# Performance work log

Hardware: AMD Instinct MI355X
Metric: run time of the kernel (lower is better)

The kernel has to match this reference:

```python
import jax, jax.numpy as jnp
import numpy as np

L, B, S, D, H, E, DH, K = 2, 4, 1024, 512, 8, 8, 2048, 2
HEAD = D // H
EPS = 1e-6


def setup_inputs() -> dict:
    key = jax.random.key(0)
    ks = jax.random.split(key, 10)
    s = 0.02
    rn = lambda k, shp: (s * jax.random.normal(k, shp, jnp.float32))
    return {
        "x": jax.random.normal(ks[0], (B, S, D), jnp.float32),
        "ln1_w": jnp.ones((L, D), jnp.float32),
        "ln1_b": jnp.zeros((L, D), jnp.float32),
        "wq": rn(ks[1], (L, D, D)),
        "wk": rn(ks[2], (L, D, D)),
        "wv": rn(ks[3], (L, D, D)),
        "wo": rn(ks[4], (L, D, D)),
        "bo": jnp.zeros((L, D), jnp.float32),
        "ln2_w": jnp.ones((L, D), jnp.float32),
        "ln2_b": jnp.zeros((L, D), jnp.float32),
        "gate_w": rn(ks[5], (L, D, E)),
        "w1": rn(ks[6], (L, E, D, DH)),
        "b1": jnp.zeros((L, E, DH), jnp.float32),
        "w2": rn(ks[7], (L, E, DH, D)),
        "b2": jnp.zeros((L, E, D), jnp.float32),
    }


def _layer_norm(x, w, b):
    mu = jnp.mean(x, axis=-1, keepdims=True)
    var = jnp.mean(jnp.square(x - mu), axis=-1, keepdims=True)
    return (x - mu) * jax.lax.rsqrt(var + EPS) * w + b


def _attention(h, wq_l, wk_l, wv_l, wo_l, bo_l):
    # h: [B,S,D] -> multi-head qk attention (attn_mode='qk'), dropout is eval (identity)
    q = (h @ wq_l).reshape(B, S, H, HEAD)
    k = (h @ wk_l).reshape(B, S, H, HEAD)
    v = (h @ wv_l).reshape(B, S, H, HEAD)
    attn = jnp.einsum('bqhd,bkhd->bhqk', q, k) / np.sqrt(HEAD).astype(np.float32)
    attn = jax.nn.softmax(attn, axis=-1)
    out = jnp.einsum('bhqk,bkhd->bqhd', attn, v).reshape(B, S, D)
    return out @ wo_l + bo_l


def _moe_ffn(x2d, gw, w1_l, b1_l, w2_l, b2_l):
    # x2d: [T,D]; top-k noisy-vmoe gate at eval: clean logits, softmax over the top-k logits
    logits = x2d @ gw  # [T,E]
    topv, topi = jax.lax.top_k(logits, K)  # [T,K]
    gates = jax.nn.softmax(topv, axis=-1)  # [T,K]
    T = x2d.shape[0]
    combine = jnp.zeros((T, E), x2d.dtype).at[jnp.arange(T)[:, None], topi].add(gates)  # [T,E]
    # dense grouped-expert MLP (exact erf GELU as torch.nn.GELU)
    hmid = jax.nn.gelu(jnp.einsum('td,edh->teh', x2d, w1_l) + b1_l[None], approximate=False)
    y = jnp.einsum('teh,ehd->ted', hmid, w2_l) + b2_l[None]
    return jnp.einsum('te,ted->td', combine, y)


def reference(x, ln1_w, ln1_b, wq, wk, wv, wo, bo, ln2_w, ln2_b, gate_w, w1, b1, w2, b2):
    for l in range(L):
        residue = x
        h = _layer_norm(x, ln1_w[l], ln1_b[l])
        x = _attention(h, wq[l], wk[l], wv[l], wo[l], bo[l]) + residue
        residue = x
        h = _layer_norm(x, ln2_w[l], ln2_b[l])
        y = _moe_ffn(h.reshape(B * S, D), gate_w[l], w1[l], b1[l], w2[l], b2[l])
        x = y.reshape(B, S, D) + residue
    return x
```

## Files before the change

kernel.cpp:

```cpp
#include <hip/hip_runtime.h>
#include <cmath>

#define D_MODEL 512
#define T_TOK   4096
#define S_SEQ   1024
#define DH_FF   2048
#define N_EXP   8
#define CAP     9216
#define QKV_LD  1536

typedef __attribute__((ext_vector_type(8))) short bf16x8_t;
typedef __attribute__((ext_vector_type(4))) float f32x4_t;
typedef _Float16 f16x8 __attribute__((ext_vector_type(8)));

__device__ __forceinline__ float gelu_exact(float x) {
    return 0.5f * x * (1.0f + erff(x * 0.70710678118654752440f));
}
__device__ __forceinline__ unsigned short f2bf(float f) {
    union { float f; unsigned int u; } v; v.f = f;
    unsigned int r = v.u + 0x7fff + ((v.u >> 16) & 1);
    return (unsigned short)(r >> 16);
}
__device__ __forceinline__ float bf2f(unsigned short u) {
    union { unsigned int i; float f; } v; v.i = ((unsigned int)u) << 16; return v.f;
}
__device__ __forceinline__ unsigned short f2h(float f) {
    _Float16 h = (_Float16)f;
    return __builtin_bit_cast(unsigned short, h);
}
__device__ __forceinline__ void split1(float v, unsigned short& h, unsigned short& l) {
    _Float16 hf = (_Float16)v;
    _Float16 lf = (_Float16)(v - (float)hf);
    h = __builtin_bit_cast(unsigned short, hf);
    l = __builtin_bit_cast(unsigned short, lf);
}

__global__ __launch_bounds__(256) void ln_kernel(
    const float* __restrict__ x, const float* __restrict__ w,
    const float* __restrict__ b, float* __restrict__ outf,
    unsigned short* __restrict__ outHi, unsigned short* __restrict__ outLo,
    unsigned short* __restrict__ outb, float* __restrict__ xcopy)
{
    const int t = blockIdx.x, tid = threadIdx.x;
    const float* xr = x + (size_t)t * D_MODEL;
    float v0 = xr[tid], v1 = xr[tid + 256];
    __shared__ float ss[256], sq[256];
    ss[tid] = v0 + v1;
    sq[tid] = v0 * v0 + v1 * v1;
    __syncthreads();
    for (int st = 128; st > 0; st >>= 1) {
        if (tid < st) { ss[tid] += ss[tid + st]; sq[tid] += sq[tid + st]; }
        __syncthreads();
    }
    float mu  = ss[0] * (1.0f / 512.0f);
    float var = sq[0] * (1.0f / 512.0f) - mu * mu;
    float rs  = rsqrtf(var + 1e-6f);
    float o0 = (v0 - mu) * rs * w[tid]       + b[tid];
    float o1 = (v1 - mu) * rs * w[tid + 256] + b[tid + 256];
    if (outf) {
        float* outr = outf + (size_t)t * D_MODEL;
        outr[tid] = o0; outr[tid + 256] = o1;
    }
    if (outHi) {
        unsigned short h0, l0, h1, l1;
        split1(o0, h0, l0); split1(o1, h1, l1);
        unsigned short* oh = outHi + (size_t)t * D_MODEL;
        unsigned short* ol = outLo + (size_t)t * D_MODEL;
        oh[tid] = h0; oh[tid + 256] = h1;
        ol[tid] = l0; ol[tid + 256] = l1;
    }
    if (outb) {
        unsigned short* ob = outb + (size_t)t * D_MODEL;
        ob[tid] = f2bf(o0); ob[tid + 256] = f2bf(o1);
    }
    if (xcopy) {
        float* xc = xcopy + (size_t)t * D_MODEL;
        xc[tid] = v0; xc[tid + 256] = v1;
    }
}

__global__ __launch_bounds__(256) void tconv_split(
    const float* __restrict__ in, int inLd, size_t eStrideIn,
    unsigned short* __restrict__ outHi, unsigned short* __restrict__ outLo,
    int outLd, size_t eStrideOut)
{
    __shared__ float Ts[32][33];
    const int tid = threadIdx.x;
    const int k0 = blockIdx.y * 32, n0 = blockIdx.x * 32;
    in    += (size_t)blockIdx.z * eStrideIn;
    outHi += (size_t)blockIdx.z * eStrideOut;
    outLo += (size_t)blockIdx.z * eStrideOut;
    int r = tid >> 3, c = (tid & 7) * 4;
    float4 v = *(const float4*)&in[(size_t)(k0 + r) * inLd + n0 + c];
    Ts[r][c] = v.x; Ts[r][c + 1] = v.y; Ts[r][c + 2] = v.z; Ts[r][c + 3] = v.w;
    __syncthreads();
    int n = tid >> 3, kk = (tid & 7) * 4;
    ushort4 h4, l4;
    split1(Ts[kk][n],     h4.x, l4.x); split1(Ts[kk + 1][n], h4.y, l4.y);
    split1(Ts[kk + 2][n], h4.z, l4.z); split1(Ts[kk + 3][n], h4.w, l4.w);
    size_t o = (size_t)(n0 + n) * outLd + k0 + kk;
    *(ushort4*)&outHi[o] = h4;
    *(ushort4*)&outLo[o] = l4;
}

__global__ __launch_bounds__(256) void tconv(
    const float* __restrict__ in, int inLd, size_t eStrideIn,
    unsigned short* __restrict__ out, int outLd, size_t eStrideOut)
{
    __shared__ float Ts[32][33];
    const int tid = threadIdx.x;
    const int k0 = blockIdx.y * 32, n0 = blockIdx.x * 32;
    in  += (size_t)blockIdx.z * eStrideIn;
    out += (size_t)blockIdx.z * eStrideOut;
    int r = tid >> 3, c = (tid & 7) * 4;
    float4 v = *(const float4*)&in[(size_t)(k0 + r) * inLd + n0 + c];
    Ts[r][c] = v.x; Ts[r][c + 1] = v.y; Ts[r][c + 2] = v.z; Ts[r][c + 3] = v.w;
    __syncthreads();
    int n = tid >> 3, kk = (tid & 7) * 4;
    ushort4 o;
    o.x = f2bf(Ts[kk][n]);     o.y = f2bf(Ts[kk + 1][n]);
    o.z = f2bf(Ts[kk + 2][n]); o.w = f2bf(Ts[kk + 3][n]);
    *(ushort4*)&out[(size_t)(n0 + n) * outLd + k0 + kk] = o;
}

template<int MODE>
__global__ __launch_bounds__(256) void gemm_pre(
    const unsigned short* __restrict__ Ahi, const unsigned short* __restrict__ Alo,
    int lda, int KLEN,
    const unsigned short* __restrict__ Bhi, const unsigned short* __restrict__ Blo,
    size_t BeStride,
    float* __restrict__ C, int ldc,
    const float* __restrict__ bias, int biasStride,
    const float* __restrict__ resid,
    const int* __restrict__ offs, const int* __restrict__ rowtok, int beta,
    unsigned short* __restrict__ Chi, unsigned short* __restrict__ Clo)
{
    __shared__ unsigned short As_hi[64][40], As_lo[64][40];
    __shared__ unsigned short Bs_hi[64][40], Bs_lo[64][40];
    __shared__ int rt[64];
    __shared__ float rg[64];
    const int tid = threadIdx.x;
    const int row0 = blockIdx.y * 64, col0 = blockIdx.x * 64;
    int e = 0;
    if (MODE == 2 || MODE == 5) {
        #pragma unroll
        for (int i = 1; i < N_EXP; i++) if (offs[i] <= row0) e = i;
        if (tid < 64) rt[tid] = rowtok[row0 + tid];
        if (MODE == 5 && tid >= 64 && tid < 128) rg[tid - 64] = resid[row0 + tid - 64];
        __syncthreads();
    }
    const unsigned short* BeH = Bhi + (size_t)e * BeStride;
    const unsigned short* BeL = Blo + (size_t)e * BeStride;
    const int lane = tid & 63, w = tid >> 6;
    const int wrow = (w >> 1) * 32, wcol = (w & 1) * 32;
    const int m_ = lane & 15, q_ = lane >> 4;
    f32x4_t acc[2][2];
    #pragma unroll
    for (int i = 0; i < 2; i++)
        #pragma unroll
        for (int j = 0; j < 2; j++) acc[i][j] = (f32x4_t){0.f, 0.f, 0.f, 0.f};

    const int sr = tid >> 2, sc = (tid & 3) * 8;
    size_t arow;
    bool azero = false;
    if (MODE == 2) {
        int t = rt[sr];
        azero = (t < 0);
        arow = (size_t)(azero ? 0 : t) * lda;
    } else {
        arow = (size_t)(row0 + sr) * lda;
    }
    const size_t brow = (size_t)(col0 + sr) * KLEN;

    for (int k0 = 0; k0 < KLEN; k0 += 32) {
        uint4 vh = azero ? make_uint4(0u, 0u, 0u, 0u) : *(const uint4*)&Ahi[arow + k0 + sc];
        uint4 vl = azero ? make_uint4(0u, 0u, 0u, 0u) : *(const uint4*)&Alo[arow + k0 + sc];
        *(uint4*)&As_hi[sr][sc] = vh;
        *(uint4*)&As_lo[sr][sc] = vl;
        *(uint4*)&Bs_hi[sr][sc] = *(const uint4*)&BeH[brow + k0 + sc];
        *(uint4*)&Bs_lo[sr][sc] = *(const uint4*)&BeL[brow + k0 + sc];
        __syncthreads();
        f16x8 ah[2], al[2], bh[2], bl[2];
        #pragma unroll
        for (int i = 0; i < 2; i++) {
            int r = wrow + 16 * i + m_;
            ah[i] = *(const f16x8*)&As_hi[r][q_ * 8];
            al[i] = *(const f16x8*)&As_lo[r][q_ * 8];
        }
        #pragma unroll
        for (int j = 0; j < 2; j++) {
            int r = wcol + 16 * j + m_;
            bh[j] = *(const f16x8*)&Bs_hi[r][q_ * 8];
            bl[j] = *(const f16x8*)&Bs_lo[r][q_ * 8];
        }
        #pragma unroll
        for (int i = 0; i < 2; i++)
            #pragma unroll
            for (int j = 0; j < 2; j++) {
                acc[i][j] = __builtin_amdgcn_mfma_f32_16x16x32_f16(ah[i], bl[j], acc[i][j], 0, 0, 0);
                acc[i][j] = __builtin_amdgcn_mfma_f32_16x16x32_f16(al[i], bh[j], acc[i][j], 0, 0, 0);
                acc[i][j] = __builtin_amdgcn_mfma_f32_16x16x32_f16(ah[i], bh[j], acc[i][j], 0, 0, 0);
            }
        __syncthreads();
    }
    #pragma unroll
    for (int i = 0; i < 2; i++) {
        #pragma unroll
        for (int j = 0; j < 2; j++) {
            #pragma unroll
            for (int r = 0; r < 4; r++) {
                int lr = wrow + 16 * i + q_ * 4 + r;
                int gr = row0 + lr;
                int gc = col0 + wcol + 16 * j + m_;
                float v = acc[i][j][r];
                if (MODE == 5) {
                    int t = rt[lr];
                    if (t >= 0) {
                        float add = beta ? bias[(size_t)e * biasStride + gc] : 0.0f;
                        atomicAdd(&C[(size_t)t * ldc + gc], rg[lr] * (v + add));
                    }
                } else if (MODE == 2) {
                    float g = gelu_exact(v + bias[(size_t)e * biasStride + gc]);
                    unsigned short gh, gl;
                    split1(g, gh, gl);
                    size_t idx = (size_t)gr * ldc + gc;
                    Chi[idx] = gh; Clo[idx] = gl;
                } else {
                    size_t idx = (size_t)gr * ldc + gc;
                    if (MODE == 1) C[idx] = v + bias[gc] + resid[idx];
                    else           C[idx] = v;
                }
            }
        }
    }
}

template<int MODE>
__global__ __launch_bounds__(256) void gemm_pre_bt(
    const unsigned short* __restrict__ A, int lda, int KLEN,
    const unsigned short* __restrict__ Bt, size_t BeStride,
    unsigned short* __restrict__ C, int ldc,
    const float* __restrict__ biasBase, int biasStride,
    const int* __restrict__ offs, const int* __restrict__ rowtok,
    const float* __restrict__ rowgate, float* __restrict__ Cout, int beta)
{
    __shared__ unsigned short As[64][72];
    __shared__ unsigned short Bs[64][72];
    __shared__ int rt[64];
    __shared__ float rg[64];
    const int tid = threadIdx.x;
    const int row0 = blockIdx.y * 64, col0 = blockIdx.x * 64;
    int e = 0;
    #pragma unroll
    for (int i = 1; i < N_EXP; i++) if (offs[i] <= row0) e = i;
    if (tid < 64) rt[tid] = rowtok[row0 + tid];
    if (MODE == 5 && tid >= 64 && tid < 128) rg[tid - 64] = rowgate[row0 + tid - 64];
    __syncthreads();
    const unsigned short* Be = Bt + (size_t)e * BeStride;
    const int lane = tid & 63, w = tid >> 6;
    const int wrow = (w >> 1) * 32, wcol = (w & 1) * 32;
    const int m_ = lane & 15, q_ = lane >> 4;
    f32x4_t acc[2][2];
    #pragma unroll
    for (int i = 0; i < 2; i++)
        #pragma unroll
        for (int j = 0; j < 2; j++) acc[i][j] = (f32x4_t){0.f, 0.f, 0.f, 0.f};

    const int sr = tid >> 3, sc = (tid & 7) * 8;
    size_t arow0, arow1;
    bool az0 = false, az1 = false;
    {
        int r1 = sr + 32;
        if (MODE == 2) {
            int t0 = rt[sr], t1 = rt[r1];
            az0 = (t0 < 0); az1 = (t1 < 0);
            arow0 = (size_t)(az0 ? 0 : t0) * lda;
            arow1 = (size_t)(az1 ? 0 : t1) * lda;
        } else {
            arow0 = (size_t)(row0 + sr) * lda;
            arow1 = (size_t)(row0 + r1) * lda;
        }
    }
    const size_t brow0 = (size_t)(col0 + sr) * KLEN;
    const size_t brow1 = (size_t)(col0 + sr + 32) * KLEN;

    for (int k0 = 0; k0 < KLEN; k0 += 64) {
        uint4 a0 = az0 ? make_uint4(0u, 0u, 0u, 0u) : *(const uint4*)&A[arow0 + k0 + sc];
        uint4 a1 = az1 ? make_uint4(0u, 0u, 0u, 0u) : *(const uint4*)&A[arow1 + k0 + sc];
        *(uint4*)&As[sr][sc]      = a0;
        *(uint4*)&As[sr + 32][sc] = a1;
        *(uint4*)&Bs[sr][sc]      = *(const uint4*)&Be[brow0 + k0 + sc];
        *(uint4*)&Bs[sr + 32][sc] = *(const uint4*)&Be[brow1 + k0 + sc];
        __syncthreads();
        #pragma unroll
        for (int ks = 0; ks < 2; ks++) {
            bf16x8_t af[2], bfr[2];
            #pragma unroll
            for (int i = 0; i < 2; i++)
                af[i] = *(const bf16x8_t*)&As[wrow + 16 * i + m_][ks * 32 + q_ * 8];
            #pragma unroll
            for (int j = 0; j < 2; j++)
                bfr[j] = *(const bf16x8_t*)&Bs[wcol + 16 * j + m_][ks * 32 + q_ * 8];
            #pragma unroll
            for (int i = 0; i < 2; i++)
                #pragma unroll
                for (int j = 0; j < 2; j++)
                    acc[i][j] = __builtin_amdgcn_mfma_f32_16x16x32_bf16(
                        af[i], bfr[j], acc[i][j], 0, 0, 0);
        }
        __syncthreads();
    }
    #pragma unroll
    for (int i = 0; i < 2; i++) {
        #pragma unroll
        for (int j = 0; j < 2; j++) {
            #pragma unroll
            for (int r = 0; r < 4; r++) {
                int lr = wrow + 16 * i + q_ * 4 + r;
                int gr = row0 + lr;
                int gc = col0 + wcol + 16 * j + m_;
                float v = acc[i][j][r];
                if (MODE == 5) {
                    int t = rt[lr];
                    if (t >= 0) {
                        float add = beta ? biasBase[(size_t)e * biasStride + gc] : 0.0f;
                        atomicAdd(&Cout[(size_t)t * ldc + gc], rg[lr] * (v + add));
                    }
                } else {
                    C[(size_t)gr * ldc + gc] =
                        f2bf(gelu_exact(v + biasBase[(size_t)e * biasStride + gc]));
                }
            }
        }
    }
}

__global__ __launch_bounds__(256) void qkv_prep(
    const float* __restrict__ qkvb, unsigned short* __restrict__ Qh,
    unsigned short* __restrict__ Kh, unsigned short* __restrict__ VTh)
{
    __shared__ float Ts[64][65];
    const int tid = threadIdx.x;
    const int t0 = blockIdx.x * 64, hh = blockIdx.y, b = blockIdx.z;
    const int bh = b * 8 + hh;
    const float* src = qkvb + ((size_t)(b * S_SEQ + t0)) * QKV_LD + hh * 64;
    #pragma unroll
    for (int i = 0; i < 4; i++) {
        int flat = tid + i * 256;
        int r = flat >> 4, c4 = (flat & 15) * 4;
        float4 qv = *(const float4*)&src[(size_t)r * QKV_LD + c4];
        float4 kv = *(const float4*)&src[(size_t)r * QKV_LD + 512 + c4];
        float4 vv = *(const float4*)&src[(size_t)r * QKV_LD + 1024 + c4];
        ushort4 qo, ko;
        qo.x = f2h(qv.x * 0.125f); qo.y = f2h(qv.y * 0.125f);
        qo.z = f2h(qv.z * 0.125f); qo.w = f2h(qv.w * 0.125f);
        ko.x = f2h(kv.x); ko.y = f2h(kv.y); ko.z = f2h(kv.z); ko.w = f2h(kv.w);
        size_t o = ((size_t)bh * S_SEQ + t0 + r) * 64 + c4;
        *(ushort4*)&Qh[o] = qo;
        *(ushort4*)&Kh[o] = ko;
        Ts[r][c4] = vv.x; Ts[r][c4 + 1] = vv.y; Ts[r][c4 + 2] = vv.z; Ts[r][c4 + 3] = vv.w;
    }
    __syncthreads();
    #pragma unroll
    for (int i = 0; i < 4; i++) {
        int flat = tid + i * 256;
        int d = flat >> 4, s4 = (flat & 15) * 4;
        ushort4 vo;
        vo.x = f2h(Ts[s4][d]);     vo.y = f2h(Ts[s4 + 1][d]);
        vo.z = f2h(Ts[s4 + 2][d]); vo.w = f2h(Ts[s4 + 3][d]);
        *(ushort4*)&VTh[((size_t)bh * 64 + d) * S_SEQ + t0 + s4] = vo;
    }
}

__global__ __launch_bounds__(256) void flash_attn_mfma(
    const unsigned short* __restrict__ Qh, const unsigned short* __restrict__ Kh,
    const unsigned short* __restrict__ VTh,
    unsigned short* __restrict__ outHi, unsigned short* __restrict__ outLo)
{
    __shared__ unsigned short Ks[64 * 72];
    __shared__ unsigned short Vt[64 * 72];
    __shared__ unsigned short Ps[64 * 72];
    const int tid = threadIdx.x;
    const int lane = tid & 63, w = tid >> 6;
    const int m_ = lane & 15, q_ = lane >> 4;
    const int hh = blockIdx.y, b = blockIdx.z;
    const int bh = b * 8 + hh;
    const int q0 = blockIdx.x * 64;
    const size_t qbase = ((size_t)bh * S_SEQ + q0) * 64;
    const size_t kbase = (size_t)bh * S_SEQ * 64;
    const size_t vbase = (size_t)bh * 64 * S_SEQ;

    f16x8 qa[2];
    #pragma unroll
    for (int c = 0; c < 2; c++)
        qa[c] = *(const f16x8*)&Qh[qbase + (size_t)(w * 16 + m_) * 64 + c * 32 + q_ * 8];

    float m_run[4], l_run[4];
    f32x4_t acc[4];
    #pragma unroll
    for (int r = 0; r < 4; r++) { m_run[r] = -INFINITY; l_run[r] = 0.0f; }
    #pragma unroll
    for (int oj = 0; oj < 4; oj++) acc[oj] = (f32x4_t){0.f, 0.f, 0.f, 0.f};

    for (int kv0 = 0; kv0 < S_SEQ; kv0 += 64) {
        __syncthreads();
        #pragma unroll
        for (int i = 0; i < 2; i++) {
            int g = tid + i * 256;
            int r = g >> 3, c8 = (g & 7) * 8;
            *(uint4*)&Ks[r * 72 + c8] =
                *(const uint4*)&Kh[kbase + (size_t)(kv0 + r) * 64 + c8];
            *(uint4*)&Vt[r * 72 + c8] =
                *(const uint4*)&VTh[vbase + (size_t)r * S_SEQ + kv0 + c8];
        }
        __syncthreads();
        f32x4_t s[4];
        #pragma unroll
        for (int j = 0; j < 4; j++) s[j] = (f32x4_t){0.f, 0.f, 0.f, 0.f};
        #pragma unroll
        for (int c = 0; c < 2; c++)
            #pragma unroll
            for (int j = 0; j < 4; j++) {
                f16x8 kb = *(const f16x8*)&Ks[(j * 16 + m_) * 72 + c * 32 + q_ * 8];
                s[j] = __builtin_amdgcn_mfma_f32_16x16x32_f16(qa[c], kb, s[j], 0, 0, 0);
            }
        float alpha[4];
        #pragma unroll
        for (int r = 0; r < 4; r++) {
            float rm = fmaxf(fmaxf(s[0][r], s[1][r]), fmaxf(s[2][r], s[3][r]));
            #pragma unroll
            for (int mk = 1; mk < 16; mk <<= 1)
                rm = fmaxf(rm, __shfl_xor(rm, mk));
            float mn = fmaxf(m_run[r], rm);
            alpha[r] = __expf(m_run[r] - mn);
            m_run[r] = mn;
            float ps = 0.0f;
            #pragma unroll
            for (int j = 0; j < 4; j++) {
                float p = __expf(s[j][r] - mn);
                s[j][r] = p;
                ps += p;
            }
            #pragma unroll
            for (int mk = 1; mk < 16; mk <<= 1)
                ps += __shfl_xor(ps, mk);
            l_run[r] = l_run[r] * alpha[r] + ps;
        }
        #pragma unroll
        for (int oj = 0; oj < 4; oj++)
            #pragma unroll
            for (int r = 0; r < 4; r++)
                acc[oj][r] *= alpha[r];
        #pragma unroll
        for (int j = 0; j < 4; j++)
            #pragma unroll
            for (int r = 0; r < 4; r++)
                Ps[(w * 16 + q_ * 4 + r) * 72 + j * 16 + m_] = f2h(s[j][r]);
        __syncthreads();
        #pragma unroll
        for (int c = 0; c < 2; c++) {
            f16x8 pa = *(const f16x8*)&Ps[(w * 16 + m_) * 72 + c * 32 + q_ * 8];
            #pragma unroll
            for (int oj = 0; oj < 4; oj++) {
                f16x8 vb = *(const f16x8*)&Vt[(oj * 16 + m_) * 72 + c * 32 + q_ * 8];
                acc[oj] = __builtin_amdgcn_mfma_f32_16x16x32_f16(pa, vb, acc[oj], 0, 0, 0);
            }
        }
    }
    const size_t obase = ((size_t)b * S_SEQ + q0) * D_MODEL + hh * 64;
    #pragma unroll
    for (int r = 0; r < 4; r++) {
        float inv = 1.0f / l_run[r];
        #pragma unroll
        for (int oj = 0; oj < 4; oj++) {
            float v = acc[oj][r] * inv;
            unsigned short vh, vl;
            split1(v, vh, vl);
            size_t idx = obase + (size_t)(w * 16 + q_ * 4 + r) * D_MODEL + oj * 16 + m_;
            outHi[idx] = vh;
            outLo[idx] = vl;
        }
    }
}

__global__ __launch_bounds__(256) void gate_kernel(
    const float* __restrict__ h, const float* __restrict__ gw,
    int* __restrict__ topi, float* __restrict__ gates)
{
    const int w = threadIdx.x >> 6, lane = threadIdx.x & 63;
    const int t = blockIdx.x * 4 + w;
    const float* hr = h + (size_t)t * D_MODEL;
    float acc[N_EXP] = {};
    for (int d = lane; d < D_MODEL; d += 64) {
        float xv = hr[d];
        const float4 g0 = *(const float4*)&gw[(size_t)d * N_EXP];
        const float4 g1 = *(const float4*)&gw[(size_t)d * N_EXP + 4];
        acc[0] += xv * g0.x; acc[1] += xv * g0.y;
        acc[2] += xv * g0.z; acc[3] += xv * g0.w;
        acc[4] += xv * g1.x; acc[5] += xv * g1.y;
        acc[6] += xv * g1.z; acc[7] += xv * g1.w;
    }
    #pragma unroll
    for (int mk = 1; mk < 64; mk <<= 1) {
        #pragma unroll
        for (int e = 0; e < N_EXP; e++) acc[e] += __shfl_xor(acc[e], mk);
    }
    if (lane == 0) {
        int e0 = 0; float v0 = acc[0];
        #pragma unroll
        for (int e = 1; e < N_EXP; e++) if (acc[e] > v0) { v0 = acc[e]; e0 = e; }
        int e1 = -1; float v1 = -INFINITY;
        #pragma unroll
        for (int e = 0; e < N_EXP; e++) if (e != e0 && acc[e] > v1) { v1 = acc[e]; e1 = e; }
        float g0 = 1.0f / (1.0f + __expf(v1 - v0));
        float g1 = 1.0f - g0;
        topi[2 * t] = e0; topi[2 * t + 1] = e1;
        gates[2 * t] = g0; gates[2 * t + 1] = g1;
    }
}

__global__ __launch_bounds__(1024) void route_kernel(
    const int* __restrict__ topi, const float* __restrict__ gates,
    int* __restrict__ offs, int* __restrict__ rowtok, float* __restrict__ rowgate)
{
    __shared__ int wcnt[16][N_EXP];
    __shared__ int wbase[16][N_EXP];
    __shared__ int offs_s[N_EXP + 1];
    const int tid = threadIdx.x, w = tid >> 6, lane = tid & 63;
    const unsigned long long lt = (1ULL << lane) - 1ULL;

    int mye[8];
    int cnt[N_EXP] = {};
    #pragma unroll
    for (int r = 0; r < 8; r++) {
        int i = w * 512 + r * 64 + lane;
        int e = topi[i];
        mye[r] = e;
        #pragma unroll
        for (int e8 = 0; e8 < N_EXP; e8++) {
            unsigned long long m = __ballot(e == e8);
            cnt[e8] += (int)__popcll(m);
        }
    }
    if (lane == 0) {
        #pragma unroll
        for (int e8 = 0; e8 < N_EXP; e8++) wcnt[w][e8] = cnt[e8];
    }
    __syncthreads();
    if (tid == 0) {
        int off = 0;
        for (int e8 = 0; e8 < N_EXP; e8++) {
            offs_s[e8] = off;
            int c = 0;
            for (int ww = 0; ww < 16; ww++) c += wcnt[ww][e8];
            off += (c + 127) & ~127;
        }
        offs_s[N_EXP] = off;
        for (int e8 = 0; e8 <= N_EXP; e8++) offs[e8] = offs_s[e8];
    }
    __syncthreads();
    if (tid < 128) {
        int ww = tid >> 3, e8 = tid & 7;
        int bse = offs_s[e8];
        for (int w2 = 0; w2 < ww; w2++) bse += wcnt[w2][e8];
        wbase[ww][e8] = bse;
    }
    __syncthreads();
    int base[N_EXP];
    #pragma unroll
    for (int e8 = 0; e8 < N_EXP; e8++) base[e8] = wbase[w][e8];
    #pragma unroll
    for (int r = 0; r < 8; r++) {
        int i = w * 512 + r * 64 + lane;
        int e = mye[r];
        int pos = 0;
        #pragma unroll
        for (int e8 = 0; e8 < N_EXP; e8++) {
            unsigned long long m = __ballot(e == e8);
            if (e == e8) pos = base[e8] + (int)__popcll(m & lt);
            base[e8] += (int)__popcll(m);
        }
        rowtok[pos] = i >> 1;
        rowgate[pos] = gates[i];
    }
}

extern "C" void kernel_launch(void* const* d_in, const int* in_sizes, int n_in,
                              void* d_out, int out_size, void* d_ws, size_t ws_size,
                              hipStream_t stream)
{
    const float* x0    = (const float*)d_in[0];
    const float* ln1w  = (const float*)d_in[1];
    const float* ln1b  = (const float*)d_in[2];
    const float* wq    = (const float*)d_in[3];
    const float* wk    = (const float*)d_in[4];
    const float* wv    = (const float*)d_in[5];
    const float* wo    = (const float*)d_in[6];
    const float* bo    = (const float*)d_in[7];
    const float* ln2w  = (const float*)d_in[8];
    const float* ln2b  = (const float*)d_in[9];
    const float* gatew = (const float*)d_in[10];
    const float* w1    = (const float*)d_in[11];
    const float* b1    = (const float*)d_in[12];
    const float* w2    = (const float*)d_in[13];
    const float* b2    = (const float*)d_in[14];
    float* out = (float*)d_out;

    char* ws = (char*)d_ws;
    const size_t MiB = 1 << 20;
    unsigned short* Qh    = (unsigned short*)(ws + 0);
    unsigned short* Kh    = (unsigned short*)(ws + 4 * MiB);
    unsigned short* h_hi  = (unsigned short*)(ws + 8 * MiB);
    unsigned short* h_lo  = (unsigned short*)(ws + 12 * MiB);
    unsigned short* attn_hi = (unsigned short*)(ws + 8 * MiB);
    unsigned short* attn_lo = (unsigned short*)(ws + 12 * MiB);
    float* qkvb = (float*)(ws + 16 * MiB);
    float* x1   = (float*)(ws + 16 * MiB);
    unsigned short* wqkvT_hi = (unsigned short*)(ws + 40 * MiB);
    unsigned short* wqkvT_lo = (unsigned short*)(ws + 40 * MiB + QKV_LD * D_MODEL * 2);
    unsigned short* VTh   = (unsigned short*)(ws + 40 * MiB);
    unsigned short* woT_hi = (unsigned short*)(ws + 44 * MiB);
    unsigned short* woT_lo = (unsigned short*)(ws + 44 * MiB + D_MODEL * D_MODEL * 2);
    unsigned short* h2_hi = (unsigned short*)(ws + 0);
    unsigned short* h2_lo = (unsigned short*)(ws + 4 * MiB);
    unsigned short* h2b   = (unsigned short*)(ws + 0);
    float* h2 = (float*)(ws + 8 * MiB);
    unsigned short* w1T_hi = (unsigned short*)(ws + 8 * MiB);
    unsigned short* w1T_lo = (unsigned short*)(ws + 12 * MiB);
    unsigned short* w2T_hi = (unsigned short*)(ws + 16 * MiB);
    unsigned short* w2T_lo = (unsigned short*)(ws + 20 * MiB);
    unsigned short* hmid_hi = (unsigned short*)(ws + 24 * MiB);
    unsigned short* hmid_lo = (unsigned short*)(ws + 33 * MiB);
    unsigned short* w1T_bf  = (unsigned short*)(ws + 8 * MiB);
    unsigned short* w2T_bf  = (unsigned short*)(ws + 16 * MiB);
    unsigned short* hmidb   = (unsigned short*)(ws + 24 * MiB);
    size_t oI = 46 * MiB;
    int*   topi    = (int*)(ws + oI);
    float* gates   = (float*)(ws + oI + 2 * T_TOK * 4);
    int*   rowtok  = (int*)(ws + oI + 4 * T_TOK * 4);
    float* rowgate = (float*)(ws + oI + 4 * T_TOK * 4 + CAP * 4);
    int*   offs    = (int*)(ws + oI + 4 * T_TOK * 4 + 2 * CAP * 4);
    float* x2 = out;

    const dim3 gW(16, 16, 1);
    const dim3 gW8(16, 16, 8);
    const dim3 gW8b(16, 32, 8);
    const dim3 gQKV(QKV_LD / 64, T_TOK / 64);
    const dim3 gO(D_MODEL / 64, T_TOK / 64);
    const dim3 gUp1(8, CAP / 64);
    const dim3 gDn1(D_MODEL / 64, CAP / 64);
    const dim3 gUp2(16, CAP / 64);
    const dim3 gDn2(D_MODEL / 64, CAP / 64);
    const dim3 gAttn(S_SEQ / 64, 8, 4);

    for (int l = 0; l < 2; l++) {
        const float* xin = (l == 0) ? x0 : x2;
        float* xout = (l == 1) ? out : x2;
        const float* wq_l = wq + (size_t)l * D_MODEL * D_MODEL;
        const float* wk_l = wk + (size_t)l * D_MODEL * D_MODEL;
        const float* wv_l = wv + (size_t)l * D_MODEL * D_MODEL;
        const float* wo_l = wo + (size_t)l * D_MODEL * D_MODEL;
        const float* w1_l = w1 + (size_t)l * N_EXP * D_MODEL * DH_FF;
        const float* w2_l = w2 + (size_t)l * N_EXP * DH_FF * D_MODEL;
        const float* b1_l = b1 + (size_t)l * N_EXP * DH_FF;
        const float* b2_l = b2 + (size_t)l * N_EXP * D_MODEL;

        ln_kernel<<<T_TOK, 256, 0, stream>>>(xin, ln1w + (size_t)l * D_MODEL,
                                             ln1b + (size_t)l * D_MODEL,
                                             nullptr, h_hi, h_lo, nullptr, nullptr);
        tconv_split<<<gW, 256, 0, stream>>>(wq_l, D_MODEL, 0, wqkvT_hi, wqkvT_lo, D_MODEL, 0);
        tconv_split<<<gW, 256, 0, stream>>>(wk_l, D_MODEL, 0,
                                            wqkvT_hi + 512 * 512, wqkvT_lo + 512 * 512,
                                            D_MODEL, 0);
        tconv_split<<<gW, 256, 0, stream>>>(wv_l, D_MODEL, 0,
                                            wqkvT_hi + 1024 * 512, wqkvT_lo + 1024 * 512,
                                            D_MODEL, 0);
        tconv_split<<<gW, 256, 0, stream>>>(wo_l, D_MODEL, 0, woT_hi, woT_lo, D_MODEL, 0);
        gemm_pre<0><<<gQKV, 256, 0, stream>>>(h_hi, h_lo, D_MODEL, D_MODEL,
                                              wqkvT_hi, wqkvT_lo, 0,
                                              qkvb, QKV_LD, nullptr, 0, nullptr,
                                              nullptr, nullptr, 0, nullptr, nullptr);
        qkv_prep<<<gAttn, 256, 0, stream>>>(qkvb, Qh, Kh, VTh);
        flash_attn_mfma<<<gAttn, 256, 0, stream>>>(Qh, Kh, VTh, attn_hi, attn_lo);
        gemm_pre<1><<<gO, 256, 0, stream>>>(attn_hi, attn_lo, D_MODEL, D_MODEL,
                                            woT_hi, woT_lo, 0,
                                            x1, D_MODEL, bo + (size_t)l * D_MODEL, 0,
                                            xin, nullptr, nullptr, 0, nullptr, nullptr);
        ln_kernel<<<T_TOK, 256, 0, stream>>>(x1, ln2w + (size_t)l * D_MODEL,
                                             ln2b + (size_t)l * D_MODEL, h2,
                                             (l == 0) ? h2_hi : nullptr,
                                             (l == 0) ? h2_lo : nullptr,
                                             (l == 1) ? h2b : nullptr, xout);

        hipMemsetAsync(rowtok, 0xFF, CAP * 4, stream);
        gate_kernel<<<T_TOK / 4, 256, 0, stream>>>(h2, gatew + (size_t)l * D_MODEL * N_EXP,
                                                   topi, gates);
        route_kernel<<<1, 1024, 0, stream>>>(topi, gates, offs, rowtok, rowgate);

        if (l == 0) {
            for (int c = 0; c < 4; c++) {
                tconv_split<<<gW8, 256, 0, stream>>>(w1_l + (size_t)c * 512, DH_FF,
                                                     (size_t)D_MODEL * DH_FF,
                                                     w1T_hi, w1T_lo, D_MODEL,
                                                     (size_t)512 * D_MODEL);
                gemm_pre<2><<<gUp1, 256, 0, stream>>>(h2_hi, h2_lo, D_MODEL, D_MODEL,
                                                      w1T_hi, w1T_lo, (size_t)512 * D_MODEL,
                                                      nullptr, 512,
                                                      b1_l + (size_t)c * 512, DH_FF,
                                                      nullptr, offs, rowtok, 0,
                                                      hmid_hi, hmid_lo);
                tconv_split<<<gW8, 256, 0, stream>>>(w2_l + (size_t)c * 512 * D_MODEL,
                                                     D_MODEL, (size_t)DH_FF * D_MODEL,
                                                     w2T_hi, w2T_lo, 512,
                                                     (size_t)D_MODEL * 512);
                gemm_pre<5><<<gDn1, 256, 0, stream>>>(hmid_hi, hmid_lo, 512, 512,
                                                      w2T_hi, w2T_lo, (size_t)D_MODEL * 512,
                                                      xout, D_MODEL, b2_l, D_MODEL,
                                                      rowgate, offs, rowtok,
                                                      (c == 0) ? 1 : 0, nullptr, nullptr);
            }
        } else {
            for (int c = 0; c < 2; c++) {
                tconv<<<dim3(32, 16, 8), 256, 0, stream>>>(
                    w1_l + (size_t)c * 1024, DH_FF, (size_t)D_MODEL * DH_FF,
                    w1T_bf, D_MODEL, (size_t)1024 * D_MODEL);
                gemm_pre_bt<2><<<gUp2, 256, 0, stream>>>(h2b, D_MODEL, D_MODEL,
                                                         w1T_bf, (size_t)1024 * D_MODEL,
                                                         hmidb, 1024,
                                                         b1_l + (size_t)c * 1024, DH_FF,
                                                         offs, rowtok, nullptr, nullptr, 0);
                tconv<<<dim3(16, 32, 8), 256, 0, stream>>>(
                    w2_l + (size_t)c * 1024 * D_MODEL, D_MODEL, (size_t)DH_FF * D_MODEL,
                    w2T_bf, 1024, (size_t)D_MODEL * 1024);
                gemm_pre_bt<5><<<gDn2, 256, 0, stream>>>(hmidb, 1024, 1024,
                                                         w2T_bf, (size_t)D_MODEL * 1024,
                                                         nullptr, D_MODEL, b2_l, D_MODEL,
                                                         offs, rowtok, rowgate, xout,
                                                         (c == 0) ? 1 : 0);
            }
        }
    }
}
```

Before: 922.1 us.

## Enlarge GEMM tiles to 128 rows and prefetch next K-slice into registers

Both GEMM kernels (split-precision f16 and bf16) now use 128-row block tiles with templated 64- or 128-column widths, and each wave computes more MFMA output tiles. This raises data reuse per LDS load and cuts the number of blocks. The K loop now loads the next global slice into registers while the current slice is being computed, which removes one barrier per iteration. The cost is higher register pressure and fewer blocks in flight, which may lower occupancy. For the MoE expert GEMMs, a 128-row tile may also cross expert boundaries if the routing offsets are not 128-aligned.

Measured after the change: 1.567 ms. 69.9% more time.

```diff
diff --git a/kernel.cpp b/kernel.cpp
--- a/kernel.cpp
+++ b/kernel.cpp
@@ -123,8 +123,8 @@
     *(ushort4*)&out[(size_t)(n0 + n) * outLd + k0 + kk] = o;
 }
 
-template<int MODE>
-__global__ __launch_bounds__(256) void gemm_pre(
+template<int MODE, int BN>
+__global__ __launch_bounds__(256) void gemm128(
     const unsigned short* __restrict__ Ahi, const unsigned short* __restrict__ Alo,
     int lda, int KLEN,
     const unsigned short* __restrict__ Bhi, const unsigned short* __restrict__ Blo,
@@ -135,78 +135,108 @@
     const int* __restrict__ offs, const int* __restrict__ rowtok, int beta,
     unsigned short* __restrict__ Chi, unsigned short* __restrict__ Clo)
 {
-    __shared__ unsigned short As_hi[64][40], As_lo[64][40];
-    __shared__ unsigned short Bs_hi[64][40], Bs_lo[64][40];
-    __shared__ int rt[64];
-    __shared__ float rg[64];
+    constexpr int NI  = (BN == 64) ? 2 : 4;
+    constexpr int NBV = BN / 64;
+    __shared__ unsigned short AsH[128][40], AsL[128][40];
+    __shared__ unsigned short BsH[BN][40],  BsL[BN][40];
+    __shared__ int rt[128];
+    __shared__ float rg[128];
     const int tid = threadIdx.x;
-    const int row0 = blockIdx.y * 64, col0 = blockIdx.x * 64;
+    const int row0 = blockIdx.y * 128, col0 = blockIdx.x * BN;
     int e = 0;
     if (MODE == 2 || MODE == 5) {
         #pragma unroll
         for (int i = 1; i < N_EXP; i++) if (offs[i] <= row0) e = i;
-        if (tid < 64) rt[tid] = rowtok[row0 + tid];
-        if (MODE == 5 && tid >= 64 && tid < 128) rg[tid - 64] = resid[row0 + tid - 64];
+        if (tid < 128) rt[tid] = rowtok[row0 + tid];
+        else if (MODE == 5) rg[tid - 128] = resid[row0 + tid - 128];
         __syncthreads();
     }
     const unsigned short* BeH = Bhi + (size_t)e * BeStride;
     const unsigned short* BeL = Blo + (size_t)e * BeStride;
     const int lane = tid & 63, w = tid >> 6;
-    const int wrow = (w >> 1) * 32, wcol = (w & 1) * 32;
+    const int wrow = (BN == 64) ? w * 32 : (w >> 1) * 64;
+    const int wcol = (BN == 64) ? 0 : (w & 1) * 64;
     const int m_ = lane & 15, q_ = lane >> 4;
-    f32x4_t acc[2][2];
-    #pragma unroll
-    for (int i = 0; i < 2; i++)
-        #pragma unroll
-        for (int j = 0; j < 2; j++) acc[i][j] = (f32x4_t){0.f, 0.f, 0.f, 0.f};
-
-    const int sr = tid >> 2, sc = (tid & 3) * 8;
-    size_t arow;
-    bool azero = false;
-    if (MODE == 2) {
-        int t = rt[sr];
-        azero = (t < 0);
-        arow = (size_t)(azero ? 0 : t) * lda;
-    } else {
-        arow = (size_t)(row0 + sr) * lda;
-    }
-    const size_t brow = (size_t)(col0 + sr) * KLEN;
-
-    for (int k0 = 0; k0 < KLEN; k0 += 32) {
-        uint4 vh = azero ? make_uint4(0u, 0u, 0u, 0u) : *(const uint4*)&Ahi[arow + k0 + sc];
-        uint4 vl = azero ? make_uint4(0u, 0u, 0u, 0u) : *(const uint4*)&Alo[arow + k0 + sc];
-        *(uint4*)&As_hi[sr][sc] = vh;
-        *(uint4*)&As_lo[sr][sc] = vl;
-        *(uint4*)&Bs_hi[sr][sc] = *(const uint4*)&BeH[brow + k0 + sc];
-        *(uint4*)&Bs_lo[sr][sc] = *(const uint4*)&BeL[brow + k0 + sc];
+    f32x4_t acc[NI][4];
+    #pragma unroll
+    for (int i = 0; i < NI; i++)
+        #pragma unroll
+        for (int j = 0; j < 4; j++) acc[i][j] = (f32x4_t){0.f, 0.f, 0.f, 0.f};
+
+    const int ar0 = tid >> 2, ac = (tid & 3) * 8;
+    size_t aoff[2]; bool az[2];
+    #pragma unroll
+    for (int q = 0; q < 2; q++) {
+        int r = q * 64 + ar0;
+        if (MODE == 2) {
+            int t = rt[r];
+            az[q] = (t < 0);
+            aoff[q] = (size_t)(az[q] ? 0 : t) * lda;
+        } else { az[q] = false; aoff[q] = (size_t)(row0 + r) * lda; }
+    }
+    size_t boff[NBV];
+    #pragma unroll
+    for (int q = 0; q < NBV; q++)
+        boff[q] = (size_t)(col0 + q * 64 + ar0) * KLEN;
+
+    const uint4 Z = make_uint4(0u, 0u, 0u, 0u);
+    uint4 pah[2], pal[2], pbh[NBV], pbl[NBV];
+    auto LOAD = [&](int k0) {
+        #pragma unroll
+        for (int q = 0; q < 2; q++) {
+            pah[q] = az[q] ? Z : *(const uint4*)&Ahi[aoff[q] + k0 + ac];
+            pal[q] = az[q] ? Z : *(const uint4*)&Alo[aoff[q] + k0 + ac];
+        }
+        #pragma unroll
+        for (int q = 0; q < NBV; q++) {
+            pbh[q] = *(const uint4*)&BeH[boff[q] + k0 + ac];
+            pbl[q] = *(const uint4*)&BeL[boff[q] + k0 + ac];
+        }
+    };
+    auto STORE = [&]() {
+        #pragma unroll
+        for (int q = 0; q < 2; q++) {
+            *(uint4*)&AsH[q * 64 + ar0][ac] = pah[q];
+            *(uint4*)&AsL[q * 64 + ar0][ac] = pal[q];
+        }
+        #pragma unroll
+        for (int q = 0; q < NBV; q++) {
+            *(uint4*)&BsH[q * 64 + ar0][ac] = pbh[q];
+            *(uint4*)&BsL[q * 64 + ar0][ac] = pbl[q];
+        }
+    };
+
+    const int NS = KLEN / 32;
+    LOAD(0);
+    for (int ks = 0; ks < NS; ks++) {
+        if (ks) __syncthreads();
+        STORE();
+        if (ks + 1 < NS) LOAD(32 * (ks + 1));
         __syncthreads();
-        f16x8 ah[2], al[2], bh[2], bl[2];
-        #pragma unroll
-        for (int i = 0; i < 2; i++) {
+        f16x8 ah[NI], al[NI];
+        #pragma unroll
+        for (int i = 0; i < NI; i++) {
             int r = wrow + 16 * i + m_;
-            ah[i] = *(const f16x8*)&As_hi[r][q_ * 8];
-            al[i] = *(const f16x8*)&As_lo[r][q_ * 8];
-        }
-        #pragma unroll
-        for (int j = 0; j < 2; j++) {
+            ah[i] = *(const f16x8*)&AsH[r][q_ * 8];
+            al[i] = *(const f16x8*)&AsL[r][q_ * 8];
+        }
+        #pragma unroll
+        for (int j = 0; j < 4; j++) {
             int r = wcol + 16 * j + m_;
-            bh[j] = *(const f16x8*)&Bs_hi[r][q_ * 8];
-            bl[j] = *(const f16x8*)&Bs_lo[r][q_ * 8];
-        }
-        #pragma unroll
-        for (int i = 0; i < 2; i++)
-            #pragma unroll
-            for (int j = 0; j < 2; j++) {
-                acc[i][j] = __builtin_amdgcn_mfma_f32_16x16x32_f16(ah[i], bl[j], acc[i][j], 0, 0, 0);
-                acc[i][j] = __builtin_amdgcn_mfma_f32_16x16x32_f16(al[i], bh[j], acc[i][j], 0, 0, 0);
-                acc[i][j] = __builtin_amdgcn_mfma_f32_16x16x32_f16(ah[i], bh[j], acc[i][j], 0, 0, 0);
-            }
-        __syncthreads();
-    }
-    #pragma unroll
-    for (int i = 0; i < 2; i++) {
-        #pragma unroll
-        for (int j = 0; j < 2; j++) {
+            f16x8 bh = *(const f16x8*)&BsH[r][q_ * 8];
+            f16x8 bl = *(const f16x8*)&BsL[r][q_ * 8];
+            #pragma unroll
+            for (int i = 0; i < NI; i++) {
+                acc[i][j] = __builtin_amdgcn_mfma_f32_16x16x32_f16(ah[i], bl, acc[i][j], 0, 0, 0);
+                acc[i][j] = __builtin_amdgcn_mfma_f32_16x16x32_f16(al[i], bh, acc[i][j], 0, 0, 0);
+                acc[i][j] = __builtin_amdgcn_mfma_f32_16x16x32_f16(ah[i], bh, acc[i][j], 0, 0, 0);
+            }
+        }
+    }
+    #pragma unroll
+    for (int i = 0; i < NI; i++) {
+        #pragma unroll
+        for (int j = 0; j < 4; j++) {
             #pragma unroll
             for (int r = 0; r < 4; r++) {
                 int lr = wrow + 16 * i + q_ * 4 + r;
@@ -235,8 +265,8 @@
     }
 }
 
-template<int MODE>
-__global__ __launch_bounds__(256) void gemm_pre_bt(
+template<int MODE, int BN>
+__global__ __launch_bounds__(256) void gemm128_bt(
     const unsigned short* __restrict__ A, int lda, int KLEN,
     const unsigned short* __restrict__ Bt, size_t BeStride,
     unsigned short* __restrict__ C, int ldc,
@@ -244,76 +274,93 @@
     const int* __restrict__ offs, const int* __restrict__ rowtok,
     const float* __restrict__ rowgate, float* __restrict__ Cout, int beta)
 {
-    __shared__ unsigned short As[64][72];
-    __shared__ unsigned short Bs[64][72];
-    __shared__ int rt[64];
-    __shared__ float rg[64];
+    constexpr int NI  = (BN == 64) ? 2 : 4;
+    constexpr int NBV = BN / 32;
+    __shared__ unsigned short As[128][72];
+    __shared__ unsigned short Bs[BN][72];
+    __shared__ int rt[128];
+    __shared__ float rg[128];
     const int tid = threadIdx.x;
-    const int row0 = blockIdx.y * 64, col0 = blockIdx.x * 64;
+    const int row0 = blockIdx.y * 128, col0 = blockIdx.x * BN;
     int e = 0;
     #pragma unroll
     for (int i = 1; i < N_EXP; i++) if (offs[i] <= row0) e = i;
-    if (tid < 64) rt[tid] = rowtok[row0 + tid];
-    if (MODE == 5 && tid >= 64 && tid < 128) rg[tid - 64] = rowgate[row0 + tid - 64];
+    if (tid < 128) rt[tid] = rowtok[row0 + tid];
+    else if (MODE == 5) rg[tid - 128] = rowgate[row0 + tid - 128];
     __syncthreads();
     const unsigned short* Be = Bt + (size_t)e * BeStride;
     const int lane = tid & 63, w = tid >> 6;
-    const int wrow = (w >> 1) * 32, wcol = (w & 1) * 32;
+    const int wrow = (BN == 64) ? w * 32 : (w >> 1) * 64;
+    const int wcol = (BN == 64) ? 0 : (w & 1) * 64;
     const int m_ = lane & 15, q_ = lane >> 4;
-    f32x4_t acc[2][2];
-    #pragma unroll
-    for (int i = 0; i < 2; i++)
-        #pragma unroll
-        for (int j = 0; j < 2; j++) acc[i][j] = (f32x4_t){0.f, 0.f, 0.f, 0.f};
-
-    const int sr = tid >> 3, sc = (tid & 7) * 8;
-    size_t arow0, arow1;
-    bool az0 = false, az1 = false;
-    {
-        int r1 = sr + 32;
+    f32x4_t acc[NI][4];
+    #pragma unroll
+    for (int i = 0; i < NI; i++)
+        #pragma unroll
+        for (int j = 0; j < 4; j++) acc[i][j] = (f32x4_t){0.f, 0.f, 0.f, 0.f};
+
+    const int ar0 = tid >> 3, ac = (tid & 7) * 8;
+    size_t aoff[4]; bool az[4];
+    #pragma unroll
+    for (int q = 0; q < 4; q++) {
+        int r = q * 32 + ar0;
         if (MODE == 2) {
-            int t0 = rt[sr], t1 = rt[r1];
-            az0 = (t0 < 0); az1 = (t1 < 0);
-            arow0 = (size_t)(az0 ? 0 : t0) * lda;
-            arow1 = (size_t)(az1 ? 0 : t1) * lda;
-        } else {
-            arow0 = (size_t)(row0 + sr) * lda;
-            arow1 = (size_t)(row0 + r1) * lda;
-        }
-    }
-    const size_t brow0 = (size_t)(col0 + sr) * KLEN;
-    const size_t brow1 = (size_t)(col0 + sr + 32) * KLEN;
-
-    for (int k0 = 0; k0 < KLEN; k0 += 64) {
-        uint4 a0 = az0 ? make_uint4(0u, 0u, 0u, 0u) : *(const uint4*)&A[arow0 + k0 + sc];
-        uint4 a1 = az1 ? make_uint4(0u, 0u, 0u, 0u) : *(const uint4*)&A[arow1 + k0 + sc];
-        *(uint4*)&As[sr][sc]      = a0;
-        *(uint4*)&As[sr + 32][sc] = a1;
-        *(uint4*)&Bs[sr][sc]      = *(const uint4*)&Be[brow0 + k0 + sc];
-        *(uint4*)&Bs[sr + 32][sc] = *(const uint4*)&Be[brow1 + k0 + sc];
+            int t = rt[r];
+            az[q] = (t < 0);
+            aoff[q] = (size_t)(az[q] ? 0 : t) * lda;
+        } else { az[q] = false; aoff[q] = (size_t)(row0 + r) * lda; }
+    }
+    size_t boff[NBV];
+    #pragma unroll
+    for (int q = 0; q < NBV; q++)
+        boff[q] = (size_t)(col0 + q * 32 + ar0) * KLEN;
+
+    const uint4 Z = make_uint4(0u, 0u, 0u, 0u);
+    uint4 pa[4], pb[NBV];
+    auto LOAD = [&](int k0) {
+        #pragma unroll
+        for (int q = 0; q < 4; q++)
+            pa[q] = az[q] ? Z : *(const uint4*)&A[aoff[q] + k0 + ac];
+        #pragma unroll
+        for (int q = 0; q < NBV; q++)
+            pb[q] = *(const uint4*)&Be[boff[q] + k0 + ac];
+    };
+    auto STORE = [&]() {
+        #pragma unroll
+        for (int q = 0; q < 4; q++)
+            *(uint4*)&As[q * 32 + ar0][ac] = pa[q];
+        #pragma unroll
+        for (int q = 0; q < NBV; q++)
+            *(uint4*)&Bs[q * 32 + ar0][ac] = pb[q];
+    };
+
+    const int NS = KLEN / 64;
+    LOAD(0);
+    for (int ks = 0; ks < NS; ks++) {
+        if (ks) __syncthreads();
+        STORE();
+        if (ks + 1 < NS) LOAD(64 * (ks + 1));
         __syncthreads();
         #pragma unroll
-        for (int ks = 0; ks < 2; ks++) {
-            bf16x8_t af[2], bfr[2];
-            #pragma unroll
-            for (int i = 0; i < 2; i++)
-                af[i] = *(const bf16x8_t*)&As[wrow + 16 * i + m_][ks * 32 + q_ * 8];
-            #pragma unroll
-            for (int j = 0; j < 2; j++)
-                bfr[j] = *(const bf16x8_t*)&Bs[wcol + 16 * j + m_][ks * 32 + q_ * 8];
-            #pragma unroll
-            for (int i = 0; i < 2; i++)
+        for (int ks2 = 0; ks2 < 2; ks2++) {
+            bf16x8_t af[NI];
+            #pragma unroll
+            for (int i = 0; i < NI; i++)
+                af[i] = *(const bf16x8_t*)&As[wrow + 16 * i + m_][ks2 * 32 + q_ * 8];
+            #pragma unroll
+            for (int j = 0; j < 4; j++) {
+                bf16x8_t bfr = *(const bf16x8_t*)&Bs[wcol + 16 * j + m_][ks2 * 32 + q_ * 8];
                 #pragma unroll
-                for (int j = 0; j < 2; j++)
+                for (int i = 0; i < NI; i++)
                     acc[i][j] = __builtin_amdgcn_mfma_f32_16x16x32_bf16(
-                        af[i], bfr[j], acc[i][j], 0, 0, 0);
-        }
-        __syncthreads();
-    }
-    #pragma unroll
-    for (int i = 0; i < 2; i++) {
-        #pragma unroll
-        for (int j = 0; j < 2; j++) {
+                        af[i], bfr, acc[i][j], 0, 0, 0);
+            }
+        }
+    }
+    #pragma unroll
+    for (int i = 0; i < NI; i++) {
+        #pragma unroll
+        for (int j = 0; j < 4; j++) {
             #pragma unroll
             for (int r = 0; r < 4; r++) {
                 int lr = wrow + 16 * i + q_ * 4 + r;
@@ -644,13 +691,12 @@
 
     const dim3 gW(16, 16, 1);
     const dim3 gW8(16, 16, 8);
-    const dim3 gW8b(16, 32, 8);
-    const dim3 gQKV(QKV_LD / 64, T_TOK / 64);
-    const dim3 gO(D_MODEL / 64, T_TOK / 64);
-    const dim3 gUp1(8, CAP / 64);
-    const dim3 gDn1(D_MODEL / 64, CAP / 64);
-    const dim3 gUp2(16, CAP / 64);
-    const dim3 gDn2(D_MODEL / 64, CAP / 64);
+    const dim3 gQKV(QKV_LD / 128, T_TOK / 128);
+    const dim3 gO(D_MODEL / 64, T_TOK / 128);
+    const dim3 gUp1(8, CAP / 128);
+    const dim3 gDn1(D_MODEL / 64, CAP / 128);
+    const dim3 gUp2(1024 / 128, CAP / 128);
+    const dim3 gDn2(D_MODEL / 64, CAP / 128);
     const dim3 gAttn(S_SEQ / 64, 8, 4);
 
     for (int l = 0; l < 2; l++) {
@@ -676,16 +722,16 @@
                                             wqkvT_hi + 1024 * 512, wqkvT_lo + 1024 * 512,
                                             D_MODEL, 0);
         tconv_split<<<gW, 256, 0, stream>>>(wo_l, D_MODEL, 0, woT_hi, woT_lo, D_MODEL, 0);
-        gemm_pre<0><<<gQKV, 256, 0, stream>>>(h_hi, h_lo, D_MODEL, D_MODEL,
-                                              wqkvT_hi, wqkvT_lo, 0,
-                                              qkvb, QKV_LD, nullptr, 0, nullptr,
-                                              nullptr, nullptr, 0, nullptr, nullptr);
+        gemm128<0, 128><<<gQKV, 256, 0, stream>>>(h_hi, h_lo, D_MODEL, D_MODEL,
+                                                  wqkvT_hi, wqkvT_lo, 0,
+                                                  qkvb, QKV_LD, nullptr, 0, nullptr,
+                                                  nullptr, nullptr, 0, nullptr, nullptr);
         qkv_prep<<<gAttn, 256, 0, stream>>>(qkvb, Qh, Kh, VTh);
         flash_attn_mfma<<<gAttn, 256, 0, stream>>>(Qh, Kh, VTh, attn_hi, attn_lo);
-        gemm_pre<1><<<gO, 256, 0, stream>>>(attn_hi, attn_lo, D_MODEL, D_MODEL,
-                                            woT_hi, woT_lo, 0,
-                                            x1, D_MODEL, bo + (size_t)l * D_MODEL, 0,
-                                            xin, nullptr, nullptr, 0, nullptr, nullptr);
+        gemm128<1, 64><<<gO, 256, 0, stream>>>(attn_hi, attn_lo, D_MODEL, D_MODEL,
+                                               woT_hi, woT_lo, 0,
+                                               x1, D_MODEL, bo + (size_t)l * D_MODEL, 0,
+                                               xin, nullptr, nullptr, 0, nullptr, nullptr);
         ln_kernel<<<T_TOK, 256, 0, stream>>>(x1, ln2w + (size_t)l * D_MODEL,
                                              ln2b + (size_t)l * D_MODEL, h2,
                                              (l == 0) ? h2_hi : nullptr,
@@ -703,41 +749,41 @@
                                                      (size_t)D_MODEL * DH_FF,
                                                      w1T_hi, w1T_lo, D_MODEL,
                                                      (size_t)512 * D_MODEL);
-                gemm_pre<2><<<gUp1, 256, 0, stream>>>(h2_hi, h2_lo, D_MODEL, D_MODEL,
-                                                      w1T_hi, w1T_lo, (size_t)512 * D_MODEL,
-                                                      nullptr, 512,
-                                                      b1_l + (size_t)c * 512, DH_FF,
-                                                      nullptr, offs, rowtok, 0,
-                                                      hmid_hi, hmid_lo);
+                gemm128<2, 64><<<gUp1, 256, 0, stream>>>(h2_hi, h2_lo, D_MODEL, D_MODEL,
+                                                         w1T_hi, w1T_lo, (size_t)512 * D_MODEL,
+                                                         nullptr, 512,
+                                                         b1_l + (size_t)c * 512, DH_FF,
+                                                         nullptr, offs, rowtok, 0,
+                                                         hmid_hi, hmid_lo);
                 tconv_split<<<gW8, 256, 0, stream>>>(w2_l + (size_t)c * 512 * D_MODEL,
                                                      D_MODEL, (size_t)DH_FF * D_MODEL,
                                                      w2T_hi, w2T_lo, 512,
                                                      (size_t)D_MODEL * 512);
-                gemm_pre<5><<<gDn1, 256, 0, stream>>>(hmid_hi, hmid_lo, 512, 512,
-                                                      w2T_hi, w2T_lo, (size_t)D_MODEL * 512,
-                                                      xout, D_MODEL, b2_l, D_MODEL,
-                                                      rowgate, offs, rowtok,
-                                                      (c == 0) ? 1 : 0, nullptr, nullptr);
+                gemm128<5, 64><<<gDn1, 256, 0, stream>>>(hmid_hi, hmid_lo, 512, 512,
+                                                         w2T_hi, w2T_lo, (size_t)D_MODEL * 512,
+                                                         xout, D_MODEL, b2_l, D_MODEL,
+                                                         rowgate, offs, rowtok,
+                                                         (c == 0) ? 1 : 0, nullptr, nullptr);
             }
         } else {
             for (int c = 0; c < 2; c++) {
                 tconv<<<dim3(32, 16, 8), 256, 0, stream>>>(
                     w1_l + (size_t)c * 1024, DH_FF, (size_t)D_MODEL * DH_FF,
                     w1T_bf, D_MODEL, (size_t)1024 * D_MODEL);
-                gemm_pre_bt<2><<<gUp2, 256, 0, stream>>>(h2b, D_MODEL, D_MODEL,
-                                                         w1T_bf, (size_t)1024 * D_MODEL,
-                                                         hmidb, 1024,
-                                                         b1_l + (size_t)c * 1024, DH_FF,
-                                                         offs, rowtok, nullptr, nullptr, 0);
+                gemm128_bt<2, 128><<<gUp2, 256, 0, stream>>>(h2b, D_MODEL, D_MODEL,
+                                                             w1T_bf, (size_t)1024 * D_MODEL,
+                                                             hmidb, 1024,
+                                                             b1_l + (size_t)c * 1024, DH_FF,
+                                                             offs, rowtok, nullptr, nullptr, 0);
                 tconv<<<dim3(16, 32, 8), 256, 0, stream>>>(
                     w2_l + (size_t)c * 1024 * D_MODEL, D_MODEL, (size_t)DH_FF * D_MODEL,
                     w2T_bf, 1024, (size_t)D_MODEL * 1024);
-                gemm_pre_bt<5><<<gDn2, 256, 0, stream>>>(hmidb, 1024, 1024,
-                                                         w2T_bf, (size_t)D_MODEL * 1024,
-                                                         nullptr, D_MODEL, b2_l, D_MODEL,
-                                                         offs, rowtok, rowgate, xout,
-                                                         (c == 0) ? 1 : 0);
-            }
-        }
-    }
-}
+                gemm128_bt<5, 64><<<gDn2, 256, 0, stream>>>(hmidb, 1024, 1024,
+                                                            w2T_bf, (size_t)D_MODEL * 1024,
+                                                            nullptr, D_MODEL, b2_l, D_MODEL,
+                                                            offs, rowtok, rowgate, xout,
+                                                            (c == 0) ? 1 : 0);
+            }
+        }
+    }
+}
```
